# Performance work log

Hardware: AMD Instinct MI355X
Metric: run time of the kernel (lower is better)

## Reference

```python
import jax, jax.numpy as jnp
import numpy as np

N = 1 << 20          # query points
K = 1024             # kernels per spatial dim (regular grid)
NK = K * K
LC_DIM = 20          # n_hidden_fl
HG_LEVELS = (16, 2048)
HIDDEN = 64
OUT = 3
_CORNERS = jnp.array([[0, 0], [0, 1], [1, 0], [1, 1]], dtype=jnp.int32)


def _hashgrid(x, tables):
    # multi-level dense-grid (non-hashed; both levels fit under 2**24) bilinear lookup
    feats = []
    for res, tab in zip(HG_LEVELS, tables):
        pos = x * (res - 1)                                   # [N,2]
        i0 = jnp.clip(jnp.floor(pos).astype(jnp.int32), 0, res - 2)
        f = pos - i0.astype(x.dtype)                          # [N,2] fractional
        ci = i0[:, None, :] + _CORNERS[None]                  # [N,4,2]
        w = jnp.prod(jnp.where(_CORNERS[None] == 1, f[:, None, :], 1.0 - f[:, None, :]), axis=-1)  # [N,4]
        idx = ci[..., 0] * res + ci[..., 1]                   # [N,4]
        feats.append(jnp.einsum('nc,ncd->nd', w, tab[idx]))
    return jnp.concatenate(feats, axis=-1)                    # [N,4]


def _rbf_interp(x, kc0, ks0, lc0):
    # nearest 4 kernels = corners of the regular-grid cell containing x
    g = x * (K - 1)
    i0 = jnp.clip(jnp.floor(g).astype(jnp.int32), 0, K - 2)
    ci = i0[:, None, :] + _CORNERS[None]                      # [N,4,2]
    idx = ci[..., 0] * K + ci[..., 1]                         # [N,4]
    # nlin_s kernel: prod_d relu(1 - |x_d - kc_d| * ks)   (ks scalar per kernel)
    d = jnp.abs(x[:, None, :] - kc0[idx])                     # [N,4,2]
    w = jnp.prod(jax.nn.relu(1.0 - d * ks0[idx]), axis=-1)    # [N,4]
    w = w / (jnp.sum(w, axis=-1, keepdims=True) + 1e-8)       # rbf_lc0_normalize
    return jnp.einsum('nc,ncd->nd', w, lc0[idx])              # [N,20]


def _forward(x, hg0, hg1, kc0, ks0, lc0, lcb0, W0, b0, W1, b1, W2, b2, a0, a1, a2):
    h = jnp.concatenate([_rbf_interp(x, kc0, ks0, lc0), _hashgrid(x, (hg0, hg1))], axis=-1) + lcb0
    h = jax.nn.relu(a0 * (h @ W0.T + b0))
    h = jax.nn.relu(a1 * (h @ W1.T + b1))
    return a2 * (h @ W2.T + b2)


def setup_inputs() -> dict:
    key = jax.random.key(0)
    ks = jax.random.split(key, 8)
    x = jax.random.uniform(ks[0], (N, 2), jnp.float32)
    hg0 = jax.random.uniform(ks[1], (HG_LEVELS[0] ** 2, 2), jnp.float32, -0.3, 0.3)
    hg1 = jax.random.uniform(ks[2], (HG_LEVELS[1] ** 2, 2), jnp.float32, -0.3, 0.3)
    lin = jnp.linspace(0.0, 1.0, K, dtype=jnp.float32)
    gx, gy = jnp.meshgrid(lin, lin, indexing='ij')
    kc0 = jnp.stack([gx.ravel(), gy.ravel()], axis=-1)        # [NK,2] regular grid centers
    ks0 = jnp.full((NK, 1), float(K - 1), jnp.float32)        # 1/mean(side_interval)
    lc0 = jax.random.uniform(ks[3], (NK, LC_DIM), jnp.float32, -0.3, 0.3)
    din = LC_DIM + 4
    lcb0 = jnp.zeros((din,), jnp.float32)
    W0 = jax.random.normal(ks[4], (HIDDEN, din), jnp.float32) * (1.0 / np.sqrt(din))
    b0 = jnp.zeros((HIDDEN,), jnp.float32)
    W1 = jax.random.normal(ks[5], (HIDDEN, HIDDEN), jnp.float32) * (1.0 / np.sqrt(HIDDEN))
    b1 = jnp.zeros((HIDDEN,), jnp.float32)
    W2 = jax.random.normal(ks[6], (OUT, HIDDEN), jnp.float32) * (1.0 / np.sqrt(HIDDEN))
    b2 = jnp.zeros((OUT,), jnp.float32)
    a0 = jnp.ones((1,), jnp.float32)
    a1 = jnp.ones((1,), jnp.float32)
    a2 = jnp.ones((1,), jnp.float32)
    return dict(x=x, hg0=hg0, hg1=hg1, kc0=kc0, ks0=ks0, lc0=lc0, lcb0=lcb0,
                W0=W0, b0=b0, W1=W1, b1=b1, W2=W2, b2=b2, a0=a0, a1=a1, a2=a2)


def reference(x, hg0, hg1, kc0, ks0, lc0, lcb0, W0, b0, W1, b1, W2, b2, a0, a1, a2):
    return _forward(x, hg0, hg1, kc0, ks0, lc0, lcb0, W0, b0, W1, b1, W2, b2, a0, a1, a2)
```

## Files before the change

### kernel.cpp

```cpp
#include <hip/hip_runtime.h>
#include <cstddef>

#define KGRID 1024
#define LC_DIM 20
#define DIN 24
#define HIDDEN 64
#define OUT_DIM 3

typedef __attribute__((ext_vector_type(8))) short bf16x8;
typedef __attribute__((ext_vector_type(4))) float f32x4;

union FragCast { unsigned long long u[2]; bf16x8 v; short s[8]; };

__device__ inline short bf16_rne(float x) {
    unsigned u = __float_as_uint(x);
    unsigned r = (u + 0x7FFFu + ((u >> 16) & 1u)) >> 16;
    return (short)r;
}
__device__ inline float bf16f(short s) {
    return __uint_as_float(((unsigned)(unsigned short)s) << 16);
}

__device__ inline void wave_lds_fence() {
    asm volatile("s_waitcnt lgkmcnt(0)" ::: "memory");
    __builtin_amdgcn_sched_barrier(0);
}

__global__ void prep_wfrags(const float* __restrict__ W0,
                            const float* __restrict__ W1,
                            short* __restrict__ ws)
{
    const int tid = threadIdx.x;
    const int u = tid >> 6;
    const int l = tid & 63;
    const int q = l & 15;
    const int g = l >> 4;

    {
        float wv[8];
        if (g < 3) {
            const float* src = W0 + (16 * u + q) * DIN + 8 * g;
#pragma unroll
            for (int j = 0; j < 8; ++j) wv[j] = src[j];
        } else {
#pragma unroll
            for (int j = 0; j < 8; ++j) wv[j] = 0.f;
        }
        short* dh = ws + (u * 64 + l) * 8;
        short* dl = ws + 2048 + (u * 64 + l) * 8;
#pragma unroll
        for (int j = 0; j < 8; ++j) {
            const short hb = bf16_rne(wv[j]);
            dh[j] = hb;
            dl[j] = bf16_rne(wv[j] - bf16f(hb));
        }
    }

#pragma unroll
    for (int s = 0; s < 2; ++s) {
        const float* src = W1 + (16 * u + q) * HIDDEN + 32 * s + 8 * g;
        short* dh = ws + 4096 + ((s * 4 + u) * 64 + l) * 8;
        short* dl = ws + 8192 + ((s * 4 + u) * 64 + l) * 8;
#pragma unroll
        for (int j = 0; j < 8; ++j) {
            const float v = src[j];
            const short hb = bf16_rne(v);
            dh[j] = hb;
            dl[j] = bf16_rne(v - bf16f(hb));
        }
    }
}

__global__ __launch_bounds__(256, 3) void fused_rbf_mlp(
    const float* __restrict__ x,
    const float* __restrict__ hg0,
    const float* __restrict__ hg1,
    const float* __restrict__ lc0,
    const float* __restrict__ lcb0,
    const float* __restrict__ b0,
    const float* __restrict__ b1,
    const float* __restrict__ W2,
    const float* __restrict__ b2,
    const float* __restrict__ a0, const float* __restrict__ a1, const float* __restrict__ a2,
    const short* __restrict__ wsW,
    float* __restrict__ out,
    int npts)
{
    __shared__ unsigned long long tileU[4][1152];
    __shared__ float sOut[256 * OUT_DIM];

    const int tid = threadIdx.x;
    const int w = tid >> 6;
    const int l = tid & 63;
    const int q = l & 15;
    const int g = l >> 4;

    unsigned long long* Tu = &tileU[w][0];
    short* Ts = (short*)Tu;
    const int LO_S = 2304;

    int n = blockIdx.x * 256 + tid;
    const bool valid = (n < npts);
    if (!valid) n = npts - 1;

    const float2 xv = ((const float2*)x)[n];

    float feat[DIN];
#pragma unroll
    for (int d = 0; d < LC_DIM; ++d) feat[d] = 0.f;

    {
        const float gx = xv.x * (float)(KGRID - 1);
        const float gy = xv.y * (float)(KGRID - 1);
        int ix = (int)floorf(gx); ix = ix < 0 ? 0 : (ix > KGRID - 2 ? KGRID - 2 : ix);
        int iy = (int)floorf(gy); iy = iy < 0 ? 0 : (iy > KGRID - 2 ? KGRID - 2 : iy);
        float fx = gx - (float)ix; fx = fx < 0.f ? 0.f : (fx > 1.f ? 1.f : fx);
        float fy = gy - (float)iy; fy = fy < 0.f ? 0.f : (fy > 1.f ? 1.f : fy);

        float wgt[4];
        wgt[0] = (1.f - fx) * (1.f - fy);
        wgt[1] = (1.f - fx) * fy;
        wgt[2] = fx * (1.f - fy);
        wgt[3] = fx * fy;
        const float inv = 1.f / (wgt[0] + wgt[1] + wgt[2] + wgt[3] + 1e-8f);

        const int base = ix * KGRID + iy;
        const int idx[4] = { base, base + 1, base + KGRID, base + KGRID + 1 };
#pragma unroll
        for (int c = 0; c < 4; ++c) {
            const float wn = wgt[c] * inv;
            const float4* lp = (const float4*)(lc0 + (size_t)idx[c] * LC_DIM);
#pragma unroll
            for (int qq = 0; qq < 5; ++qq) {
                const float4 v = lp[qq];
                feat[qq * 4 + 0] += wn * v.x;
                feat[qq * 4 + 1] += wn * v.y;
                feat[qq * 4 + 2] += wn * v.z;
                feat[qq * 4 + 3] += wn * v.w;
            }
        }
    }

    {
        float px = xv.x * 15.f, py = xv.y * 15.f;
        int ix = (int)floorf(px); ix = ix < 0 ? 0 : (ix > 14 ? 14 : ix);
        int iy = (int)floorf(py); iy = iy < 0 ? 0 : (iy > 14 ? 14 : iy);
        float fx = px - (float)ix, fy = py - (float)iy;
        float f0 = 0.f, f1 = 0.f;
#pragma unroll
        for (int c = 0; c < 4; ++c) {
            const int ci = ix + (c >> 1), cj = iy + (c & 1);
            const float wv = ((c >> 1) ? fx : 1.f - fx) * ((c & 1) ? fy : 1.f - fy);
            const float2 t = ((const float2*)hg0)[ci * 16 + cj];
            f0 += wv * t.x; f1 += wv * t.y;
        }
        feat[LC_DIM + 0] = f0; feat[LC_DIM + 1] = f1;

        px = xv.x * 2047.f; py = xv.y * 2047.f;
        ix = (int)floorf(px); ix = ix < 0 ? 0 : (ix > 2046 ? 2046 : ix);
        iy = (int)floorf(py); iy = iy < 0 ? 0 : (iy > 2046 ? 2046 : iy);
        fx = px - (float)ix; fy = py - (float)iy;
        f0 = 0.f; f1 = 0.f;
#pragma unroll
        for (int c = 0; c < 4; ++c) {
            const int ci = ix + (c >> 1), cj = iy + (c & 1);
            const float wv = ((c >> 1) ? fx : 1.f - fx) * ((c & 1) ? fy : 1.f - fy);
            const float2 t = ((const float2*)hg1)[ci * 2048 + cj];
            f0 += wv * t.x; f1 += wv * t.y;
        }
        feat[LC_DIM + 2] = f0; feat[LC_DIM + 3] = f1;
    }

#pragma unroll
    for (int d = 0; d < DIN; ++d) feat[d] += lcb0[d];

    const float A0 = a0[0], A1 = a1[0], A2 = a2[0];

    {
        unsigned long long rowh[8], rowl[8];
        short* rh = (short*)rowh; short* rl = (short*)rowl;
#pragma unroll
        for (int k = 0; k < DIN; ++k) {
            short hb = bf16_rne(feat[k]);
            rh[k] = hb;
            rl[k] = bf16_rne(feat[k] - bf16f(hb));
        }
#pragma unroll
        for (int k = DIN; k < 32; ++k) { rh[k] = 0; rl[k] = 0; }
#pragma unroll
        for (int i = 0; i < 8; ++i) {
            Tu[l * 9 + i] = rowh[i];
            Tu[576 + l * 9 + i] = rowl[i];
        }
    }

    const bf16x8* wsB0h = (const bf16x8*)(wsW);
    const bf16x8* wsB0l = (const bf16x8*)(wsW + 2048);
    bf16x8 B0h[4], B0l[4];
#pragma unroll
    for (int u = 0; u < 4; ++u) {
        B0h[u] = wsB0h[u * 64 + l];
        B0l[u] = wsB0l[u * 64 + l];
    }

    wave_lds_fence();

    f32x4 accA[4][4];
#pragma unroll
    for (int u = 0; u < 4; ++u) {
        const float bb = b0[16 * u + q];
#pragma unroll
        for (int t = 0; t < 4; ++t) accA[t][u] = (f32x4){bb, bb, bb, bb};
    }
#pragma unroll
    for (int u = 0; u < 4; ++u) {
#pragma unroll
        for (int t = 0; t < 4; ++t) {
            FragCast ah, al;
            const int row = 16 * t + q;
            ah.u[0] = Tu[row * 9 + 2 * g];       ah.u[1] = Tu[row * 9 + 2 * g + 1];
            al.u[0] = Tu[576 + row * 9 + 2 * g]; al.u[1] = Tu[576 + row * 9 + 2 * g + 1];
            accA[t][u] = __builtin_amdgcn_mfma_f32_16x16x32_bf16(ah.v, B0h[u], accA[t][u], 0, 0, 0);
            accA[t][u] = __builtin_amdgcn_mfma_f32_16x16x32_bf16(ah.v, B0l[u], accA[t][u], 0, 0, 0);
            accA[t][u] = __builtin_amdgcn_mfma_f32_16x16x32_bf16(al.v, B0h[u], accA[t][u], 0, 0, 0);
        }
    }

    f32x4 accB[4][4];
#pragma unroll
    for (int u = 0; u < 4; ++u) {
        const float bb = b1[16 * u + q];
#pragma unroll
        for (int t = 0; t < 4; ++t) accB[t][u] = (f32x4){bb, bb, bb, bb};
    }

    const bf16x8* wsB1h = (const bf16x8*)(wsW + 4096);
    const bf16x8* wsB1l = (const bf16x8*)(wsW + 8192);

#pragma unroll
    for (int s = 0; s < 2; ++s) {
        wave_lds_fence();
#pragma unroll
        for (int uu = 0; uu < 2; ++uu) {
            const int u = 2 * s + uu;
#pragma unroll
            for (int t = 0; t < 4; ++t) {
#pragma unroll
                for (int r = 0; r < 4; ++r) {
                    float h = accA[t][u][r] * A0;
                    h = h > 0.f ? h : 0.f;
                    const short hb = bf16_rne(h);
                    const short lb = bf16_rne(h - bf16f(hb));
                    const int m = 16 * t + 4 * g + r;
                    Ts[m * 36 + 16 * uu + q] = hb;
                    Ts[LO_S + m * 36 + 16 * uu + q] = lb;
                }
            }
        }
        wave_lds_fence();
#pragma unroll
        for (int u = 0; u < 4; ++u) {
            const bf16x8 bh = wsB1h[(s * 4 + u) * 64 + l];
            const bf16x8 bl = wsB1l[(s * 4 + u) * 64 + l];
#pragma unroll
            for (int t = 0; t < 4; ++t) {
                FragCast ah, al;
                const int row = 16 * t + q;
                ah.u[0] = Tu[row * 9 + 2 * g];       ah.u[1] = Tu[row * 9 + 2 * g + 1];
                al.u[0] = Tu[576 + row * 9 + 2 * g]; al.u[1] = Tu[576 + row * 9 + 2 * g + 1];
                accB[t][u] = __builtin_amdgcn_mfma_f32_16x16x32_bf16(ah.v, bh, accB[t][u], 0, 0, 0);
                accB[t][u] = __builtin_amdgcn_mfma_f32_16x16x32_bf16(ah.v, bl, accB[t][u], 0, 0, 0);
                accB[t][u] = __builtin_amdgcn_mfma_f32_16x16x32_bf16(al.v, bh, accB[t][u], 0, 0, 0);
            }
        }
    }

    {
        float w2v[3][4], b2v[3];
#pragma unroll
        for (int c = 0; c < 3; ++c) {
            b2v[c] = b2[c];
#pragma unroll
            for (int u = 0; u < 4; ++u) w2v[c][u] = W2[c * HIDDEN + 16 * u + q];
        }
#pragma unroll
        for (int t = 0; t < 4; ++t) {
#pragma unroll
            for (int r = 0; r < 4; ++r) {
                float hv[4];
#pragma unroll
                for (int u = 0; u < 4; ++u) {
                    float h = accB[t][u][r] * A1;
                    hv[u] = h > 0.f ? h : 0.f;
                }
                float p0 = 0.f, p1 = 0.f, p2 = 0.f;
#pragma unroll
                for (int u = 0; u < 4; ++u) {
                    p0 += w2v[0][u] * hv[u];
                    p1 += w2v[1][u] * hv[u];
                    p2 += w2v[2][u] * hv[u];
                }
#pragma unroll
                for (int mk = 1; mk < 16; mk <<= 1) {
                    p0 += __shfl_xor(p0, mk);
                    p1 += __shfl_xor(p1, mk);
                    p2 += __shfl_xor(p2, mk);
                }
                if (q == 0) {
                    const int pl = w * 64 + 16 * t + 4 * g + r;
                    sOut[pl * 3 + 0] = A2 * (p0 + b2v[0]);
                    sOut[pl * 3 + 1] = A2 * (p1 + b2v[1]);
                    sOut[pl * 3 + 2] = A2 * (p2 + b2v[2]);
                }
            }
        }
    }

    __syncthreads();
    const int blockBase = blockIdx.x * 256;
    const int nValid = npts - blockBase;
    if (nValid >= 256) {
        const int gbase = blockBase * OUT_DIM;
#pragma unroll
        for (int k = 0; k < OUT_DIM; ++k)
            out[gbase + k * 256 + tid] = sOut[k * 256 + tid];
    } else if (valid) {
#pragma unroll
        for (int k = 0; k < OUT_DIM; ++k)
            out[(blockBase + tid) * OUT_DIM + k] = sOut[tid * OUT_DIM + k];
    }
}

extern "C" void kernel_launch(void* const* d_in, const int* in_sizes, int n_in,
                              void* d_out, int out_size, void* d_ws, size_t ws_size,
                              hipStream_t stream) {
    const float* x    = (const float*)d_in[0];
    const float* hg0  = (const float*)d_in[1];
    const float* hg1  = (const float*)d_in[2];
    const float* lc0  = (const float*)d_in[5];
    const float* lcb0 = (const float*)d_in[6];
    const float* W0   = (const float*)d_in[7];
    const float* b0   = (const float*)d_in[8];
    const float* W1   = (const float*)d_in[9];
    const float* b1   = (const float*)d_in[10];
    const float* W2   = (const float*)d_in[11];
    const float* b2   = (const float*)d_in[12];
    const float* a0   = (const float*)d_in[13];
    const float* a1   = (const float*)d_in[14];
    const float* a2   = (const float*)d_in[15];

    short* wsW = (short*)d_ws;

    prep_wfrags<<<1, 256, 0, stream>>>(W0, W1, wsW);

    const int npts = in_sizes[0] / 2;
    const int grid = (npts + 255) / 256;
    fused_rbf_mlp<<<grid, 256, 0, stream>>>(x, hg0, hg1, lc0, lcb0,
                                            b0, b1, W2, b2, a0, a1, a2,
                                            wsW, (float*)d_out, npts);
}
```

Baseline: 322.1 us.

## Bucket-sort query points by spatial tile before fused RBF-MLP kernel

```diff
diff --git a/kernel.cpp b/kernel.cpp
--- a/kernel.cpp
+++ b/kernel.cpp
@@ -6,6 +6,12 @@
 #define DIN 24
 #define HIDDEN 64
 #define OUT_DIM 3
+#define NBUCKET 4096
+
+#define WS_WF_OFF   64
+#define WS_HIST_OFF 24832
+#define WS_OFFW_OFF 41472
+#define WS_SXY_OFF  58112
 
 typedef __attribute__((ext_vector_type(8))) short bf16x8;
 typedef __attribute__((ext_vector_type(4))) float f32x4;
@@ -26,11 +32,18 @@
     __builtin_amdgcn_sched_barrier(0);
 }
 
-__global__ void prep_wfrags(const float* __restrict__ W0,
-                            const float* __restrict__ W1,
-                            short* __restrict__ ws)
-{
-    const int tid = threadIdx.x;
+__device__ inline int bucket_of(float2 p) {
+    float gx = p.x * (float)(KGRID - 1);
+    float gy = p.y * (float)(KGRID - 1);
+    int ix = (int)floorf(gx); ix = ix < 0 ? 0 : (ix > KGRID - 2 ? KGRID - 2 : ix);
+    int iy = (int)floorf(gy); iy = iy < 0 ? 0 : (iy > KGRID - 2 ? KGRID - 2 : iy);
+    return (ix >> 4) * 64 + (iy >> 4);
+}
+
+__device__ inline void wfrag_prep_body(const float* __restrict__ W0,
+                                       const float* __restrict__ W1,
+                                       short* __restrict__ ws, int tid)
+{
     const int u = tid >> 6;
     const int l = tid & 63;
     const int q = l & 15;
@@ -71,8 +84,67 @@
     }
 }
 
+__global__ void hist_kernel(const float2* __restrict__ x, int npts,
+                            unsigned* __restrict__ hist)
+{
+    int i = blockIdx.x * blockDim.x + threadIdx.x;
+    const int stride = gridDim.x * blockDim.x;
+    for (; i < npts; i += stride)
+        atomicAdd(&hist[bucket_of(x[i])], 1u);
+}
+
+__global__ void scan_prep(const unsigned* __restrict__ hist,
+                          unsigned* __restrict__ offw,
+                          const float* __restrict__ W0,
+                          const float* __restrict__ W1,
+                          short* __restrict__ wf)
+{
+    __shared__ unsigned ssum[256];
+    const int t = threadIdx.x;
+    unsigned loc[16];
+    unsigned s = 0;
+#pragma unroll
+    for (int j = 0; j < 16; ++j) { loc[j] = s; s += hist[t * 16 + j]; }
+    ssum[t] = s;
+    __syncthreads();
+    for (int off = 1; off < 256; off <<= 1) {
+        unsigned v = (t >= off) ? ssum[t - off] : 0u;
+        __syncthreads();
+        ssum[t] += v;
+        __syncthreads();
+    }
+    const unsigned base = (t == 0) ? 0u : ssum[t - 1];
+#pragma unroll
+    for (int j = 0; j < 16; ++j) offw[t * 16 + j] = base + loc[j];
+
+    wfrag_prep_body(W0, W1, wf, t);
+}
+
+__global__ void scatter_kernel(const float2* __restrict__ x, int npts,
+                               unsigned* __restrict__ offw,
+                               float2* __restrict__ sxy,
+                               unsigned* __restrict__ sidx)
+{
+    int i = blockIdx.x * blockDim.x + threadIdx.x;
+    const int stride = gridDim.x * blockDim.x;
+    for (; i < npts; i += stride) {
+        const float2 p = x[i];
+        const unsigned pos = atomicAdd(&offw[bucket_of(p)], 1u);
+        sxy[pos] = p;
+        sidx[pos] = (unsigned)i;
+    }
+}
+
+__global__ void prep_wfrags(const float* __restrict__ W0,
+                            const float* __restrict__ W1,
+                            unsigned char* __restrict__ wsb)
+{
+    wfrag_prep_body(W0, W1, (short*)(wsb + WS_WF_OFF), threadIdx.x);
+}
+
 __global__ __launch_bounds__(256, 3) void fused_rbf_mlp(
-    const float* __restrict__ x,
+    const float2* __restrict__ sxy,
+    const unsigned* __restrict__ sidx,
     const float* __restrict__ hg0,
     const float* __restrict__ hg1,
     const float* __restrict__ lc0,
@@ -87,7 +159,6 @@
     int npts)
 {
     __shared__ unsigned long long tileU[4][1152];
-    __shared__ float sOut[256 * OUT_DIM];
 
     const int tid = threadIdx.x;
     const int w = tid >> 6;
@@ -99,11 +170,12 @@
     short* Ts = (short*)Tu;
     const int LO_S = 2304;
 
-    int n = blockIdx.x * 256 + tid;
+    const int blockBase = blockIdx.x * 256;
+    int n = blockBase + tid;
     const bool valid = (n < npts);
     if (!valid) n = npts - 1;
 
-    const float2 xv = ((const float2*)x)[n];
+    const float2 xv = sxy[n];
 
     float feat[DIN];
 #pragma unroll
@@ -308,26 +380,16 @@
                 }
                 if (q == 0) {
                     const int pl = w * 64 + 16 * t + 4 * g + r;
-                    sOut[pl * 3 + 0] = A2 * (p0 + b2v[0]);
-                    sOut[pl * 3 + 1] = A2 * (p1 + b2v[1]);
-                    sOut[pl * 3 + 2] = A2 * (p2 + b2v[2]);
+                    const int spos = blockBase + pl;
+                    if (spos < npts) {
+                        const int oidx = sidx ? (int)sidx[spos] : spos;
+                        out[oidx * 3 + 0] = A2 * (p0 + b2v[0]);
+                        out[oidx * 3 + 1] = A2 * (p1 + b2v[1]);
+                        out[oidx * 3 + 2] = A2 * (p2 + b2v[2]);
+                    }
                 }
             }
         }
-    }
-
-    __syncthreads();
-    const int blockBase = blockIdx.x * 256;
-    const int nValid = npts - blockBase;
-    if (nValid >= 256) {
-        const int gbase = blockBase * OUT_DIM;
-#pragma unroll
-        for (int k = 0; k < OUT_DIM; ++k)
-            out[gbase + k * 256 + tid] = sOut[k * 256 + tid];
-    } else if (valid) {
-#pragma unroll
-        for (int k = 0; k < OUT_DIM; ++k)
-            out[(blockBase + tid) * OUT_DIM + k] = sOut[tid * OUT_DIM + k];
     }
 }
 
@@ -349,13 +411,29 @@
     const float* a1   = (const float*)d_in[14];
     const float* a2   = (const float*)d_in[15];
 
-    short* wsW = (short*)d_ws;
-
-    prep_wfrags<<<1, 256, 0, stream>>>(W0, W1, wsW);
-
+    unsigned char* ws = (unsigned char*)d_ws;
+    const short* wsW  = (const short*)(ws + WS_WF_OFF);
     const int npts = in_sizes[0] / 2;
     const int grid = (npts + 255) / 256;
-    fused_rbf_mlp<<<grid, 256, 0, stream>>>(x, hg0, hg1, lc0, lcb0,
-                                            b0, b1, W2, b2, a0, a1, a2,
-                                            wsW, (float*)d_out, npts);
-}
+
+    const size_t need = (size_t)WS_SXY_OFF + (size_t)npts * 12u;
+    if (ws_size >= need) {
+        unsigned* hist = (unsigned*)(ws + WS_HIST_OFF);
+        unsigned* offw = (unsigned*)(ws + WS_OFFW_OFF);
+        float2*   sxy  = (float2*)(ws + WS_SXY_OFF);
+        unsigned* sidx = (unsigned*)(ws + WS_SXY_OFF + (size_t)npts * 8u);
+
+        hipMemsetAsync(hist, 0, NBUCKET * sizeof(unsigned), stream);
+        hist_kernel<<<1024, 256, 0, stream>>>((const float2*)x, npts, hist);
+        scan_prep<<<1, 256, 0, stream>>>(hist, offw, W0, W1, (short*)(ws + WS_WF_OFF));
+        scatter_kernel<<<1024, 256, 0, stream>>>((const float2*)x, npts, offw, sxy, sidx);
+        fused_rbf_mlp<<<grid, 256, 0, stream>>>(sxy, sidx, hg0, hg1, lc0,
+                                                lcb0, b0, b1, W2, b2, a0, a1, a2,
+                                                wsW, (float*)d_out, npts);
+    } else {
+        prep_wfrags<<<1, 256, 0, stream>>>(W0, W1, ws);
+        fused_rbf_mlp<<<grid, 256, 0, stream>>>((const float2*)x, nullptr, hg0, hg1, lc0,
+                                                lcb0, b0, b1, W2, b2, a0, a1, a2,
+                                                wsW, (float*)d_out, npts);
+    }
+}
```

Result: slower. 433.6 us (+34.6%).
